# Kernel tuning notes

Hardware: AMD Instinct MI355X
Metric: run time of the kernel (lower is better)

## Reference

```python
import jax, jax.numpy as jnp
import numpy as np

B, S, D, NH, E, H, NT, K = 32, 512, 1024, 16, 16, 256, 8, 8
LN_EPS = 1e-5
W_MI = 5e-4


def setup_inputs() -> dict:
    key = jax.random.key(0)
    ks = jax.random.split(key, 12)
    p = lambda k, shape: jax.random.normal(k, shape, dtype=jnp.float32) * 0.02
    inp = {}
    inp["tgt"] = jax.random.normal(ks[0], (B, S, D), dtype=jnp.float32)
    inp["memory"] = jax.random.normal(ks[1], (B, S, D), dtype=jnp.float32)  # unused in norm_first path (faithful to source)
    inp["ln1_g"] = jnp.ones((D,), jnp.float32)
    inp["ln1_b"] = jnp.zeros((D,), jnp.float32)
    inp["ln3_g"] = jnp.ones((D,), jnp.float32)
    inp["ln3_b"] = jnp.zeros((D,), jnp.float32)
    inp["in_proj_w"] = p(ks[2], (3 * D, D))
    inp["in_proj_b"] = jnp.zeros((3 * D,), jnp.float32)
    inp["out_proj_w"] = p(ks[3], (D, D))
    inp["out_proj_b"] = jnp.zeros((D,), jnp.float32)
    inp["gate_w"] = p(ks[4], (NT, D, E))  # per-task gating Linear (no bias)
    inp["w1"] = p(ks[5], (E, D, H))
    inp["b1"] = jnp.zeros((E, H), jnp.float32)
    inp["w2"] = p(ks[6], (E, H, D))
    inp["b2"] = jnp.zeros((E, D), jnp.float32)
    inp["task_id"] = 3
    return inp


def _ln(x, g, b):
    m = x.mean(-1, keepdims=True)
    v = jnp.mean((x - m) ** 2, -1, keepdims=True)
    return (x - m) * jax.lax.rsqrt(v + LN_EPS) * g + b


def reference(tgt, memory, ln1_g, ln1_b, ln3_g, ln3_b, in_proj_w, in_proj_b,
              out_proj_w, out_proj_b, gate_w, w1, b1, w2, b2, task_id):
    dh = D // NH
    # --- pre-LN self-attention block ---
    h = _ln(tgt, ln1_g, ln1_b)
    qkv = h @ in_proj_w.T + in_proj_b  # [B,S,3D]
    q, k, v = jnp.split(qkv, 3, axis=-1)
    q = q.reshape(B, S, NH, dh)
    k = k.reshape(B, S, NH, dh)
    v = v.reshape(B, S, NH, dh)
    scores = jnp.einsum('bqhd,bkhd->bhqk', q, k) / jnp.sqrt(jnp.float32(dh))
    attn = jax.nn.softmax(scores, axis=-1)
    ctx = jnp.einsum('bhqk,bkhd->bqhd', attn, v).reshape(B, S, D)
    x = tgt + (ctx @ out_proj_w.T + out_proj_b)

    # --- task-conditioned MoE FFN (TaskMoE: per-task gate, top-k, GELU experts) ---
    h3 = _ln(x, ln3_g, ln3_b).reshape(B * S, D)  # [T,D]
    logits = h3 @ gate_w[task_id]  # [T,E]
    probs = jax.nn.softmax(logits, axis=-1)
    top_v, top_i = jax.lax.top_k(probs, K)
    gates = top_v / (top_v.sum(-1, keepdims=True) + 1e-6)
    gate_dense = jnp.einsum('tke,tk->te', jax.nn.one_hot(top_i, E, dtype=probs.dtype), gates)  # [T,E]
    u = jax.nn.gelu(jnp.einsum('td,edh->teh', h3, w1) + b1, approximate=False)  # [T,E,H]
    uw = u * gate_dense[:, :, None]
    moe = jnp.einsum('teh,ehd->td', uw, w2) + gate_dense @ b2  # [T,D]
    x = x + moe.reshape(B, S, D)

    mean_p = probs.mean(0)
    aux_loss = W_MI * jnp.sum(mean_p * jnp.log(mean_p + 1e-6))
    return (x, aux_loss, probs.reshape(B, S, E))
```

## Files before the change

kernel.cpp:

```cpp
#include <hip/hip_runtime.h>

typedef float f32x4 __attribute__((ext_vector_type(4)));
typedef _Float16 half_t;
typedef _Float16 h8 __attribute__((ext_vector_type(8)));
typedef _Float16 h4 __attribute__((ext_vector_type(4)));

__device__ __forceinline__ f32x4 mfma16(h8 a, h8 b, f32x4 c) {
  return __builtin_amdgcn_mfma_f32_16x16x32_f16(a, b, c, 0, 0, 0);
}

__global__ __launch_bounds__(256) void ln_fwd(const float* __restrict__ x,
                                              const float* __restrict__ g,
                                              const float* __restrict__ b,
                                              half_t* __restrict__ out) {
  const int row = blockIdx.x;
  const int tid = threadIdx.x;
  const float4 v = ((const float4*)(x + (size_t)row * 1024))[tid];
  float s = v.x + v.y + v.z + v.w;
  float q = v.x * v.x + v.y * v.y + v.z * v.z + v.w * v.w;
#pragma unroll
  for (int m = 1; m < 64; m <<= 1) { s += __shfl_xor(s, m); q += __shfl_xor(q, m); }
  __shared__ float red[8];
  const int wave = tid >> 6, lane = tid & 63;
  if (lane == 0) { red[wave] = s; red[wave + 4] = q; }
  __syncthreads();
  s = red[0] + red[1] + red[2] + red[3];
  q = red[4] + red[5] + red[6] + red[7];
  const float mean = s * (1.0f / 1024.0f);
  const float var = q * (1.0f / 1024.0f) - mean * mean;
  const float rstd = rsqrtf(var + 1e-5f);
  const float4 gv = ((const float4*)g)[tid];
  const float4 bv = ((const float4*)b)[tid];
  h4 o;
  o[0] = (half_t)((v.x - mean) * rstd * gv.x + bv.x);
  o[1] = (half_t)((v.y - mean) * rstd * gv.y + bv.y);
  o[2] = (half_t)((v.z - mean) * rstd * gv.z + bv.z);
  o[3] = (half_t)((v.w - mean) * rstd * gv.w + bv.w);
  *(h4*)(out + (size_t)row * 1024 + tid * 4) = o;
}

__global__ __launch_bounds__(256) void cvt_f2h(const float* __restrict__ in,
                                               half_t* __restrict__ out, int n) {
  const int i = (blockIdx.x * 256 + threadIdx.x) * 4;
  if (i < n) {
    const float4 v = *(const float4*)(in + i);
    h4 o = {(half_t)v.x, (half_t)v.y, (half_t)v.z, (half_t)v.w};
    *(h4*)(out + i) = o;
  }
}

__global__ __launch_bounds__(256) void tr_w1(const float* __restrict__ w1,
                                             half_t* __restrict__ w1t) {
  __shared__ float tile[32][33];
  const int e = blockIdx.z;
  const int tx = threadIdx.x & 31, ty = threadIdx.x >> 5;
  const int hh = blockIdx.x * 32 + tx;
#pragma unroll
  for (int i = 0; i < 4; ++i) {
    const int d = blockIdx.y * 32 + ty + i * 8;
    tile[ty + i * 8][tx] = w1[(size_t)e * 262144 + (size_t)d * 256 + hh];
  }
  __syncthreads();
#pragma unroll
  for (int i = 0; i < 4; ++i) {
    const int hho = blockIdx.x * 32 + ty + i * 8;
    const int k = blockIdx.y * 32 + tx;
    w1t[(size_t)(e * 256 + hho) * 1024 + k] = (half_t)tile[tx][ty + i * 8];
  }
}

__global__ __launch_bounds__(256) void tr_w2(const float* __restrict__ w2,
                                             half_t* __restrict__ w2t) {
  __shared__ float tile[32][33];
  const int e = blockIdx.z;
  const int tx = threadIdx.x & 31, ty = threadIdx.x >> 5;
  const int d_in = blockIdx.x * 32 + tx;
#pragma unroll
  for (int i = 0; i < 4; ++i) {
    const int hh = blockIdx.y * 32 + ty + i * 8;
    tile[ty + i * 8][tx] = w2[(size_t)e * 262144 + (size_t)hh * 1024 + d_in];
  }
  __syncthreads();
#pragma unroll
  for (int i = 0; i < 4; ++i) {
    const int d = blockIdx.x * 32 + ty + i * 8;
    const int hh = blockIdx.y * 32 + tx;
    w2t[(size_t)d * 4096 + e * 256 + hh] = (half_t)tile[tx][ty + i * 8];
  }
}

template <int EPI>
__global__ __launch_bounds__(512, 2) void gemm256(const half_t* __restrict__ A,
                                                  const half_t* __restrict__ Bt,
                                                  int N, int K, int nbx,
                                                  const float* __restrict__ bias,
                                                  const float* __restrict__ res,
                                                  const float* __restrict__ gd,
                                                  half_t* __restrict__ Ch,
                                                  float* __restrict__ Cf) {
  __shared__ half_t lds[2][2][256 * 64];
  const int tid = threadIdx.x;
  const int wave = tid >> 6, lane = tid & 63;
  const int l15 = lane & 15, g = lane >> 4;
  const int wr = wave >> 2, wc = wave & 3;

  const int nwg = gridDim.x;
  const int bid = blockIdx.x;
  const int swz = (bid & 7) * (nwg >> 3) + (bid >> 3);
  const int bx = swz % nbx, by = swz / nbx;

  const int NT = K >> 6;
  f32x4 acc[8][4] = {};

  auto stageAB = [&](int kt) {
    const int bt = kt & 1;
    const size_t abase = (size_t)(by * 256) * K + kt * 64;
    const size_t bbase = (size_t)(bx * 256) * K + kt * 64;
#pragma unroll
    for (int j = 0; j < 4; ++j) {
      const int c = tid + j * 512;
      const int row = c >> 3, sl = c & 7;
      const int col = (sl ^ (row & 7)) << 3;
      __builtin_amdgcn_global_load_lds(
          (const __attribute__((address_space(1))) void*)(A + abase + (size_t)row * K + col),
          (__attribute__((address_space(3))) void*)(&lds[bt][0][c * 8]), 16, 0, 0);
      __builtin_amdgcn_global_load_lds(
          (const __attribute__((address_space(1))) void*)(Bt + bbase + (size_t)row * K + col),
          (__attribute__((address_space(3))) void*)(&lds[bt][1][c * 8]), 16, 0, 0);
    }
  };

  stageAB(0);
  for (int kt = 0; kt < NT; ++kt) {
    const int bt = kt & 1;
    if (kt + 1 < NT) {
      stageAB(kt + 1);
      asm volatile("s_waitcnt vmcnt(8)" ::: "memory");
    } else {
      asm volatile("s_waitcnt vmcnt(0)" ::: "memory");
    }
    __builtin_amdgcn_s_barrier();

    h8 a0[4][2], a1[4][2], b0[2][2], b1[2][2];
#pragma unroll
    for (int m4 = 0; m4 < 4; ++m4)
#pragma unroll
      for (int kk = 0; kk < 2; ++kk) {
        const int row = wr * 128 + m4 * 16 + l15;
        const int sl = ((kk << 2) | g) ^ (row & 7);
        a0[m4][kk] = *(const h8*)(&lds[bt][0][row * 64 + sl * 8]);
      }
#pragma unroll
    for (int n2 = 0; n2 < 2; ++n2)
#pragma unroll
      for (int kk = 0; kk < 2; ++kk) {
        const int rowb0 = wc * 64 + n2 * 16 + l15;
        const int slb0 = ((kk << 2) | g) ^ (rowb0 & 7);
        b0[n2][kk] = *(const h8*)(&lds[bt][1][rowb0 * 64 + slb0 * 8]);
        const int rowb1 = wc * 64 + 32 + n2 * 16 + l15;
        const int slb1 = ((kk << 2) | g) ^ (rowb1 & 7);
        b1[n2][kk] = *(const h8*)(&lds[bt][1][rowb1 * 64 + slb1 * 8]);
      }
#pragma unroll
    for (int m4 = 0; m4 < 4; ++m4)
#pragma unroll
      for (int n2 = 0; n2 < 2; ++n2)
#pragma unroll
        for (int kk = 0; kk < 2; ++kk) {
          acc[m4][n2] = mfma16(a0[m4][kk], b0[n2][kk], acc[m4][n2]);
          acc[m4][2 + n2] = mfma16(a0[m4][kk], b1[n2][kk], acc[m4][2 + n2]);
        }
#pragma unroll
    for (int m4 = 0; m4 < 4; ++m4)
#pragma unroll
      for (int kk = 0; kk < 2; ++kk) {
        const int row = wr * 128 + 64 + m4 * 16 + l15;
        const int sl = ((kk << 2) | g) ^ (row & 7);
        a1[m4][kk] = *(const h8*)(&lds[bt][0][row * 64 + sl * 8]);
      }
#pragma unroll
    for (int m4 = 0; m4 < 4; ++m4)
#pragma unroll
      for (int n2 = 0; n2 < 2; ++n2)
#pragma unroll
        for (int kk = 0; kk < 2; ++kk) {
          acc[4 + m4][n2] = mfma16(a1[m4][kk], b0[n2][kk], acc[4 + m4][n2]);
          acc[4 + m4][2 + n2] = mfma16(a1[m4][kk], b1[n2][kk], acc[4 + m4][2 + n2]);
        }

    asm volatile("s_waitcnt lgkmcnt(0)" ::: "memory");
    __builtin_amdgcn_s_barrier();
  }

#pragma unroll
  for (int m = 0; m < 8; ++m) {
#pragma unroll
    for (int n = 0; n < 4; ++n) {
      const int col = bx * 256 + wc * 64 + n * 16 + l15;
      float bv = 0.0f;
      if constexpr (EPI != 3) bv = bias[col];
#pragma unroll
      for (int r = 0; r < 4; ++r) {
        const int row = by * 256 + wr * 128 + m * 16 + g * 4 + r;
        const float v = acc[m][n][r] + bv;
        if constexpr (EPI == 0) {
          Ch[(size_t)row * N + col] = (half_t)v;
        } else if constexpr (EPI == 1) {
          Cf[(size_t)row * N + col] = res[(size_t)row * N + col] + v;
        } else if constexpr (EPI == 2) {
          const float gel = 0.5f * v * (1.0f + erff(v * 0.70710678118f));
          Ch[(size_t)row * N + col] = (half_t)(gel * gd[row * 16 + (col >> 8)]);
        } else {
          Cf[(size_t)row * N + col] = res[(size_t)row * N + col] + v;
        }
      }
    }
  }
}

__global__ __launch_bounds__(256) void attn_fwd(const half_t* __restrict__ qkv,
                                                half_t* __restrict__ ctx) {
  const int bh = blockIdx.y;
  const int b = bh >> 4, h = bh & 15;
  const int qbase = blockIdx.x * 64;
  const int tid = threadIdx.x;
  const int wave = tid >> 6, lane = tid & 63;
  const int l15 = lane & 15, g = lane >> 4;
  __shared__ half_t K_s[2][32 * 64];
  __shared__ half_t Vt_s[2][64 * 32];
  __shared__ half_t P_s[4][16 * 32];

  const size_t qrow = (size_t)(b * 512 + qbase + wave * 16 + l15);
  h8 aq0 = *(const h8*)(qkv + qrow * 3072 + h * 64 + g * 8);
  h8 aq1 = *(const h8*)(qkv + qrow * 3072 + h * 64 + 32 + g * 8);
  aq0 = aq0 * (half_t)0.125f;
  aq1 = aq1 * (half_t)0.125f;

  float mr[4], sr[4];
  f32x4 o[4] = {};
#pragma unroll
  for (int r = 0; r < 4; ++r) { mr[r] = -1e30f; sr[r] = 0.0f; }

  const int key = tid >> 3, c0 = (tid & 7) << 3;
  const half_t* kbase = qkv + 1024 + h * 64 + c0;
  const half_t* vbase = qkv + 2048 + h * 64 + c0;

  for (int kt = 0; kt < 16; ++kt) {
    const int buf = kt & 1;
    const size_t krow = (size_t)(b * 512 + kt * 32 + key);
    const h8 kv = *(const h8*)(kbase + krow * 3072);
    *(h8*)(&K_s[buf][key * 64 + c0]) = kv;
    const h8 vv = *(const h8*)(vbase + krow * 3072);
#pragma unroll
    for (int j = 0; j < 8; ++j) Vt_s[buf][(c0 + j) * 32 + key] = vv[j];
    __syncthreads();

    f32x4 s0 = {0.f, 0.f, 0.f, 0.f}, s1 = {0.f, 0.f, 0.f, 0.f};
    s0 = mfma16(aq0, *(const h8*)(&K_s[buf][l15 * 64 + g * 8]), s0);
    s0 = mfma16(aq1, *(const h8*)(&K_s[buf][l15 * 64 + 32 + g * 8]), s0);
    s1 = mfma16(aq0, *(const h8*)(&K_s[buf][(16 + l15) * 64 + g * 8]), s1);
    s1 = mfma16(aq1, *(const h8*)(&K_s[buf][(16 + l15) * 64 + 32 + g * 8]), s1);

#pragma unroll
    for (int r = 0; r < 4; ++r) {
      const float a0 = s0[r], a1 = s1[r];
      float tm = fmaxf(a0, a1);
#pragma unroll
      for (int msk = 1; msk < 16; msk <<= 1) tm = fmaxf(tm, __shfl_xor(tm, msk));
      const float mnew = fmaxf(mr[r], tm);
      const float alpha = __expf(mr[r] - mnew);
      const float p0 = __expf(a0 - mnew), p1 = __expf(a1 - mnew);
      float rs = p0 + p1;
#pragma unroll
      for (int msk = 1; msk < 16; msk <<= 1) rs += __shfl_xor(rs, msk);
      sr[r] = sr[r] * alpha + rs;
      mr[r] = mnew;
#pragma unroll
      for (int d = 0; d < 4; ++d) o[d][r] *= alpha;
      P_s[wave][(g * 4 + r) * 32 + l15] = (half_t)p0;
      P_s[wave][(g * 4 + r) * 32 + 16 + l15] = (half_t)p1;
    }
    __syncthreads();

    const h8 pa = *(const h8*)(&P_s[wave][l15 * 32 + g * 8]);
#pragma unroll
    for (int d = 0; d < 4; ++d)
      o[d] = mfma16(pa, *(const h8*)(&Vt_s[buf][(d * 16 + l15) * 32 + g * 8]), o[d]);
  }
#pragma unroll
  for (int d = 0; d < 4; ++d) {
#pragma unroll
    for (int r = 0; r < 4; ++r) {
      const size_t row = (size_t)(b * 512 + qbase + wave * 16 + g * 4 + r);
      ctx[row * 1024 + h * 64 + d * 16 + l15] = (half_t)(o[d][r] / sr[r]);
    }
  }
}

__global__ __launch_bounds__(256) void gate_fwd(const half_t* __restrict__ h3,
                                                const float* __restrict__ gate_w,
                                                const int* __restrict__ task_id,
                                                float* __restrict__ probs,
                                                float* __restrict__ gd,
                                                float* __restrict__ mp) {
  const int tid = threadIdx.x, wave = tid >> 6, lane = tid & 63;
  const float* gw = gate_w + (size_t)task_id[0] * 16384;
  __shared__ float mp_part[16];
  if (tid < 16) mp_part[tid] = 0.0f;
  __syncthreads();
  float mpl[16];
#pragma unroll
  for (int e = 0; e < 16; ++e) mpl[e] = 0.0f;
  const int t0 = blockIdx.x * 64 + wave * 16;
  for (int tt = 0; tt < 16; ++tt) {
    const int t = t0 + tt;
    float acc[16];
#pragma unroll
    for (int e = 0; e < 16; ++e) acc[e] = 0.0f;
#pragma unroll
    for (int i = 0; i < 16; ++i) {
      const int d = i * 64 + lane;
      const float hv = (float)h3[(size_t)t * 1024 + d];
      const float4* gp = (const float4*)(gw + d * 16);
      const float4 g0 = gp[0], g1 = gp[1], g2 = gp[2], g3 = gp[3];
      acc[0] = fmaf(hv, g0.x, acc[0]);  acc[1] = fmaf(hv, g0.y, acc[1]);
      acc[2] = fmaf(hv, g0.z, acc[2]);  acc[3] = fmaf(hv, g0.w, acc[3]);
      acc[4] = fmaf(hv, g1.x, acc[4]);  acc[5] = fmaf(hv, g1.y, acc[5]);
      acc[6] = fmaf(hv, g1.z, acc[6]);  acc[7] = fmaf(hv, g1.w, acc[7]);
      acc[8] = fmaf(hv, g2.x, acc[8]);  acc[9] = fmaf(hv, g2.y, acc[9]);
      acc[10] = fmaf(hv, g2.z, acc[10]); acc[11] = fmaf(hv, g2.w, acc[11]);
      acc[12] = fmaf(hv, g3.x, acc[12]); acc[13] = fmaf(hv, g3.y, acc[13]);
      acc[14] = fmaf(hv, g3.z, acc[14]); acc[15] = fmaf(hv, g3.w, acc[15]);
    }
#pragma unroll
    for (int msk = 32; msk >= 1; msk >>= 1)
#pragma unroll
      for (int e = 0; e < 16; ++e) acc[e] += __shfl_xor(acc[e], msk);
    float mx = acc[0];
#pragma unroll
    for (int e = 1; e < 16; ++e) mx = fmaxf(mx, acc[e]);
    float p[16];
    float sum = 0.0f;
#pragma unroll
    for (int e = 0; e < 16; ++e) { p[e] = __expf(acc[e] - mx); sum += p[e]; }
    const float inv = 1.0f / sum;
#pragma unroll
    for (int e = 0; e < 16; ++e) p[e] *= inv;
    float myp = p[0];
#pragma unroll
    for (int e = 1; e < 16; ++e) myp = (lane == e) ? p[e] : myp;
    if (lane < 16) probs[(size_t)t * 16 + lane] = myp;
#pragma unroll
    for (int e = 0; e < 16; ++e) mpl[e] += p[e];
    float v[16];
#pragma unroll
    for (int e = 0; e < 16; ++e) v[e] = p[e];
    float topv[8];
    int topi[8];
#pragma unroll
    for (int k = 0; k < 8; ++k) {
      float vm = -1.0f;
      int im = 0;
#pragma unroll
      for (int e = 0; e < 16; ++e) {
        const bool gt = v[e] > vm;
        vm = gt ? v[e] : vm;
        im = gt ? e : im;
      }
      topv[k] = vm; topi[k] = im;
#pragma unroll
      for (int e = 0; e < 16; ++e) v[e] = (e == im) ? -1.0f : v[e];
    }
    float ts = 1e-6f;
#pragma unroll
    for (int k = 0; k < 8; ++k) ts += topv[k];
    const float tinv = 1.0f / ts;
    float gval = 0.0f;
#pragma unroll
    for (int k = 0; k < 8; ++k) gval = (topi[k] == lane) ? topv[k] * tinv : gval;
    if (lane < 16) gd[(size_t)t * 16 + lane] = gval;
  }
  if (lane == 0) {
#pragma unroll
    for (int e = 0; e < 16; ++e) atomicAdd(&mp_part[e], mpl[e]);
  }
  __syncthreads();
  if (tid < 16) atomicAdd(&mp[tid], mp_part[tid]);
}

__global__ void aux_fwd(const float* __restrict__ mp, float* __restrict__ out) {
  if (threadIdx.x == 0) {
    float a = 0.0f;
    for (int e = 0; e < 16; ++e) {
      const float m = mp[e] * (1.0f / 16384.0f);
      a += m * logf(m + 1e-6f);
    }
    out[0] = 5e-4f * a;
  }
}

__global__ __launch_bounds__(256) void bias2_add(const float* __restrict__ gd,
                                                 const float* __restrict__ b2,
                                                 float* __restrict__ out) {
  const int t = blockIdx.x, tid = threadIdx.x;
  __shared__ float gds[16];
  if (tid < 16) gds[tid] = gd[(size_t)t * 16 + tid];
  __syncthreads();
  float4 v = *(const float4*)(out + (size_t)t * 1024 + tid * 4);
#pragma unroll
  for (int e = 0; e < 16; ++e) {
    const float gv = gds[e];
    const float4 bv = *(const float4*)(b2 + e * 1024 + tid * 4);
    v.x = fmaf(gv, bv.x, v.x);
    v.y = fmaf(gv, bv.y, v.y);
    v.z = fmaf(gv, bv.z, v.z);
    v.w = fmaf(gv, bv.w, v.w);
  }
  *(float4*)(out + (size_t)t * 1024 + tid * 4) = v;
}

extern "C" void kernel_launch(void* const* d_in, const int* in_sizes, int n_in,
                              void* d_out, int out_size, void* d_ws, size_t ws_size,
                              hipStream_t stream) {
  const float* tgt = (const float*)d_in[0];
  const float* ln1_g = (const float*)d_in[2];
  const float* ln1_b = (const float*)d_in[3];
  const float* ln3_g = (const float*)d_in[4];
  const float* ln3_b = (const float*)d_in[5];
  const float* Wqkv = (const float*)d_in[6];
  const float* bqkv = (const float*)d_in[7];
  const float* Wout = (const float*)d_in[8];
  const float* bout = (const float*)d_in[9];
  const float* gate_w = (const float*)d_in[10];
  const float* w1 = (const float*)d_in[11];
  const float* b1 = (const float*)d_in[12];
  const float* w2 = (const float*)d_in[13];
  const float* b2 = (const float*)d_in[14];
  const int* task = (const int*)d_in[15];
  float* out = (float*)d_out;
  char* ws = (char*)d_ws;

  half_t* h = (half_t*)(ws + 0ull);
  half_t* qkv = (half_t*)(ws + 33554432ull);
  half_t* ctx = (half_t*)(ws + 134217728ull);
  half_t* uw = (half_t*)(ws + 33554432ull);
  half_t* wqkv_h = (half_t*)(ws + 167772160ull);
  half_t* wout_h = (half_t*)(ws + 174063616ull);
  half_t* w1t = (half_t*)(ws + 176160768ull);
  half_t* w2t = (half_t*)(ws + 184549376ull);
  float* gd = (float*)(ws + 192937984ull);
  float* mp = (float*)(ws + 193986560ull);

  hipMemsetAsync(mp, 0, 64, stream);
  cvt_f2h<<<3072, 256, 0, stream>>>(Wqkv, wqkv_h, 3145728);
  cvt_f2h<<<1024, 256, 0, stream>>>(Wout, wout_h, 1048576);
  tr_w1<<<dim3(8, 32, 16), 256, 0, stream>>>(w1, w1t);
  tr_w2<<<dim3(32, 8, 16), 256, 0, stream>>>(w2, w2t);

  ln_fwd<<<16384, 256, 0, stream>>>(tgt, ln1_g, ln1_b, h);
  gemm256<0><<<768, 512, 0, stream>>>(h, wqkv_h, 3072, 1024, 12, bqkv, nullptr, nullptr, qkv, nullptr);
  attn_fwd<<<dim3(8, 512), 256, 0, stream>>>(qkv, ctx);
  gemm256<1><<<256, 512, 0, stream>>>(ctx, wout_h, 1024, 1024, 4, bout, tgt, nullptr, nullptr, out);

  ln_fwd<<<16384, 256, 0, stream>>>(out, ln3_g, ln3_b, h);
  gate_fwd<<<256, 256, 0, stream>>>(h, gate_w, task, out + 16777217, gd, mp);
  aux_fwd<<<1, 64, 0, stream>>>(mp, out + 16777216);
  bias2_add<<<16384, 256, 0, stream>>>(gd, b2, out);
  gemm256<2><<<1024, 512, 0, stream>>>(h, w1t, 4096, 1024, 16, b1, nullptr, gd, uw, nullptr);
  gemm256<3><<<256, 512, 0, stream>>>(uw, w2t, 1024, 4096, 4, nullptr, out, nullptr, nullptr, out);
}
```

Baseline: 1.160 ms.

## Restructure attention with pre-transposed V, async LDS loads and larger tiles

Adds a separate kernel that transposes V per head into a contiguous buffer. Attention is rewritten to process 128 queries per block with 64-key tiles, using global_load_lds double buffering with XOR-swizzled LDS and an XCD-aware block mapping. The aim is to remove the scattered per-element V transpose stores and raise MFMA work per barrier. bias2_add now handles 16 tokens per block so the b2 loads are reused across tokens. The cost is an extra transpose pass and more register pressure in the attention kernel.

```diff
diff --git a/kernel.cpp b/kernel.cpp
--- a/kernel.cpp
+++ b/kernel.cpp
@@ -86,6 +86,27 @@
     const int d = blockIdx.x * 32 + ty + i * 8;
     const int hh = blockIdx.y * 32 + tx;
     w2t[(size_t)d * 4096 + e * 256 + hh] = (half_t)tile[tx][ty + i * 8];
+  }
+}
+
+__global__ __launch_bounds__(256) void tr_v(const half_t* __restrict__ qkv,
+                                            half_t* __restrict__ vt) {
+  __shared__ half_t tile[32][33];
+  const int bh = blockIdx.z;
+  const int b = bh >> 4, h = bh & 15;
+  const int st = blockIdx.x, dt = blockIdx.y;
+  const int tx = threadIdx.x & 31, ty = threadIdx.x >> 5;
+#pragma unroll
+  for (int i = 0; i < 4; ++i) {
+    const int s = st * 32 + ty + i * 8;
+    tile[ty + i * 8][tx] =
+        qkv[(size_t)(b * 512 + s) * 3072 + 2048 + h * 64 + dt * 32 + tx];
+  }
+  __syncthreads();
+#pragma unroll
+  for (int i = 0; i < 4; ++i) {
+    const int d = dt * 32 + ty + i * 8;
+    vt[((size_t)bh * 64 + d) * 512 + st * 32 + tx] = tile[tx][ty + i * 8];
   }
 }
 
@@ -219,82 +240,141 @@
 }
 
 __global__ __launch_bounds__(256) void attn_fwd(const half_t* __restrict__ qkv,
+                                                const half_t* __restrict__ vt,
                                                 half_t* __restrict__ ctx) {
-  const int bh = blockIdx.y;
-  const int b = bh >> 4, h = bh & 15;
-  const int qbase = blockIdx.x * 64;
+  __shared__ half_t K_s[2][64 * 64];
+  __shared__ half_t V_s[2][64 * 64];
+  __shared__ half_t P_s[4][32 * 72];
   const int tid = threadIdx.x;
   const int wave = tid >> 6, lane = tid & 63;
   const int l15 = lane & 15, g = lane >> 4;
-  __shared__ half_t K_s[2][32 * 64];
-  __shared__ half_t Vt_s[2][64 * 32];
-  __shared__ half_t P_s[4][16 * 32];
-
-  const size_t qrow = (size_t)(b * 512 + qbase + wave * 16 + l15);
-  h8 aq0 = *(const h8*)(qkv + qrow * 3072 + h * 64 + g * 8);
-  h8 aq1 = *(const h8*)(qkv + qrow * 3072 + h * 64 + 32 + g * 8);
-  aq0 = aq0 * (half_t)0.125f;
-  aq1 = aq1 * (half_t)0.125f;
-
-  float mr[4], sr[4];
-  f32x4 o[4] = {};
-#pragma unroll
-  for (int r = 0; r < 4; ++r) { mr[r] = -1e30f; sr[r] = 0.0f; }
-
-  const int key = tid >> 3, c0 = (tid & 7) << 3;
-  const half_t* kbase = qkv + 1024 + h * 64 + c0;
-  const half_t* vbase = qkv + 2048 + h * 64 + c0;
-
-  for (int kt = 0; kt < 16; ++kt) {
-    const int buf = kt & 1;
-    const size_t krow = (size_t)(b * 512 + kt * 32 + key);
-    const h8 kv = *(const h8*)(kbase + krow * 3072);
-    *(h8*)(&K_s[buf][key * 64 + c0]) = kv;
-    const h8 vv = *(const h8*)(vbase + krow * 3072);
-#pragma unroll
-    for (int j = 0; j < 8; ++j) Vt_s[buf][(c0 + j) * 32 + key] = vv[j];
-    __syncthreads();
-
-    f32x4 s0 = {0.f, 0.f, 0.f, 0.f}, s1 = {0.f, 0.f, 0.f, 0.f};
-    s0 = mfma16(aq0, *(const h8*)(&K_s[buf][l15 * 64 + g * 8]), s0);
-    s0 = mfma16(aq1, *(const h8*)(&K_s[buf][l15 * 64 + 32 + g * 8]), s0);
-    s1 = mfma16(aq0, *(const h8*)(&K_s[buf][(16 + l15) * 64 + g * 8]), s1);
-    s1 = mfma16(aq1, *(const h8*)(&K_s[buf][(16 + l15) * 64 + 32 + g * 8]), s1);
-
-#pragma unroll
-    for (int r = 0; r < 4; ++r) {
-      const float a0 = s0[r], a1 = s1[r];
-      float tm = fmaxf(a0, a1);
-#pragma unroll
-      for (int msk = 1; msk < 16; msk <<= 1) tm = fmaxf(tm, __shfl_xor(tm, msk));
-      const float mnew = fmaxf(mr[r], tm);
-      const float alpha = __expf(mr[r] - mnew);
-      const float p0 = __expf(a0 - mnew), p1 = __expf(a1 - mnew);
-      float rs = p0 + p1;
-#pragma unroll
-      for (int msk = 1; msk < 16; msk <<= 1) rs += __shfl_xor(rs, msk);
-      sr[r] = sr[r] * alpha + rs;
-      mr[r] = mnew;
-#pragma unroll
-      for (int d = 0; d < 4; ++d) o[d][r] *= alpha;
-      P_s[wave][(g * 4 + r) * 32 + l15] = (half_t)p0;
-      P_s[wave][(g * 4 + r) * 32 + 16 + l15] = (half_t)p1;
-    }
-    __syncthreads();
-
-    const h8 pa = *(const h8*)(&P_s[wave][l15 * 32 + g * 8]);
-#pragma unroll
-    for (int d = 0; d < 4; ++d)
-      o[d] = mfma16(pa, *(const h8*)(&Vt_s[buf][(d * 16 + l15) * 32 + g * 8]), o[d]);
-  }
-#pragma unroll
-  for (int d = 0; d < 4; ++d) {
-#pragma unroll
-    for (int r = 0; r < 4; ++r) {
-      const size_t row = (size_t)(b * 512 + qbase + wave * 16 + g * 4 + r);
-      ctx[row * 1024 + h * 64 + d * 16 + l15] = (half_t)(o[d][r] / sr[r]);
-    }
-  }
+
+  const int fid = blockIdx.x;
+  const int xcd = fid & 7, idx = fid >> 3;
+  const int bh = xcd * 64 + (idx >> 7) * 32 + (idx & 31);
+  const int qt = (idx >> 5) & 3;
+  const int b = bh >> 4, h = bh & 15;
+
+  h8 qreg[2][2];
+#pragma unroll
+  for (int m = 0; m < 2; ++m) {
+    const size_t qrow = (size_t)(b * 512 + qt * 128 + wave * 32 + m * 16 + l15);
+#pragma unroll
+    for (int kk = 0; kk < 2; ++kk) {
+      h8 t = *(const h8*)(qkv + qrow * 3072 + h * 64 + kk * 32 + g * 8);
+      qreg[m][kk] = t * (half_t)0.125f;
+    }
+  }
+
+  float mr[2][4], sr[2][4];
+  f32x4 o[2][4] = {};
+#pragma unroll
+  for (int m = 0; m < 2; ++m)
+#pragma unroll
+    for (int r = 0; r < 4; ++r) { mr[m][r] = -1e30f; sr[m][r] = 0.0f; }
+
+  const half_t* kg = qkv + (size_t)(b * 512) * 3072 + 1024 + h * 64;
+  const half_t* vg = vt + (size_t)bh * 32768;
+
+  auto stage = [&](int kt) {
+    const int bt = kt & 1;
+#pragma unroll
+    for (int j = 0; j < 2; ++j) {
+      const int s = tid + j * 256;
+      const int row = s >> 3, sl = s & 7;
+      const int col = (sl ^ (row & 7)) << 3;
+      __builtin_amdgcn_global_load_lds(
+          (const __attribute__((address_space(1))) void*)(kg + (size_t)(kt * 64 + row) * 3072 + col),
+          (__attribute__((address_space(3))) void*)(&K_s[bt][s * 8]), 16, 0, 0);
+      __builtin_amdgcn_global_load_lds(
+          (const __attribute__((address_space(1))) void*)(vg + (size_t)row * 512 + kt * 64 + col),
+          (__attribute__((address_space(3))) void*)(&V_s[bt][s * 8]), 16, 0, 0);
+    }
+  };
+
+  stage(0);
+  for (int kt = 0; kt < 8; ++kt) {
+    const int bt = kt & 1;
+    if (kt < 7) {
+      stage(kt + 1);
+      asm volatile("s_waitcnt vmcnt(4)" ::: "memory");
+    } else {
+      asm volatile("s_waitcnt vmcnt(0)" ::: "memory");
+    }
+    __builtin_amdgcn_s_barrier();
+
+    f32x4 s_acc[2][4] = {};
+    h8 bk[4][2];
+#pragma unroll
+    for (int n = 0; n < 4; ++n)
+#pragma unroll
+      for (int kk = 0; kk < 2; ++kk)
+        bk[n][kk] = *(const h8*)(&K_s[bt][(n * 16 + l15) * 64 + (((kk * 4 + g) ^ (l15 & 7)) << 3)]);
+#pragma unroll
+    for (int m = 0; m < 2; ++m)
+#pragma unroll
+      for (int n = 0; n < 4; ++n)
+#pragma unroll
+        for (int kk = 0; kk < 2; ++kk)
+          s_acc[m][n] = mfma16(qreg[m][kk], bk[n][kk], s_acc[m][n]);
+
+#pragma unroll
+    for (int m = 0; m < 2; ++m)
+#pragma unroll
+      for (int r = 0; r < 4; ++r) {
+        float tm = fmaxf(fmaxf(s_acc[m][0][r], s_acc[m][1][r]),
+                         fmaxf(s_acc[m][2][r], s_acc[m][3][r]));
+#pragma unroll
+        for (int msk = 1; msk < 16; msk <<= 1) tm = fmaxf(tm, __shfl_xor(tm, msk));
+        const float mnew = fmaxf(mr[m][r], tm);
+        const float al = __expf(mr[m][r] - mnew);
+        mr[m][r] = mnew;
+        float rs = 0.0f;
+#pragma unroll
+        for (int n = 0; n < 4; ++n) {
+          const float p = __expf(s_acc[m][n][r] - mnew);
+          rs += p;
+          P_s[wave][(m * 16 + g * 4 + r) * 72 + n * 16 + l15] = (half_t)p;
+        }
+#pragma unroll
+        for (int msk = 1; msk < 16; msk <<= 1) rs += __shfl_xor(rs, msk);
+        sr[m][r] = sr[m][r] * al + rs;
+#pragma unroll
+        for (int d = 0; d < 4; ++d) o[m][d][r] *= al;
+      }
+
+    h8 bv[4][2], pa[2][2];
+#pragma unroll
+    for (int n = 0; n < 4; ++n)
+#pragma unroll
+      for (int kk = 0; kk < 2; ++kk)
+        bv[n][kk] = *(const h8*)(&V_s[bt][(n * 16 + l15) * 64 + (((kk * 4 + g) ^ (l15 & 7)) << 3)]);
+#pragma unroll
+    for (int m = 0; m < 2; ++m)
+#pragma unroll
+      for (int kk = 0; kk < 2; ++kk)
+        pa[m][kk] = *(const h8*)(&P_s[wave][(m * 16 + l15) * 72 + kk * 32 + g * 8]);
+#pragma unroll
+    for (int m = 0; m < 2; ++m)
+#pragma unroll
+      for (int n = 0; n < 4; ++n)
+#pragma unroll
+        for (int kk = 0; kk < 2; ++kk)
+          o[m][n] = mfma16(pa[m][kk], bv[n][kk], o[m][n]);
+
+    asm volatile("s_waitcnt lgkmcnt(0)" ::: "memory");
+    __builtin_amdgcn_s_barrier();
+  }
+
+#pragma unroll
+  for (int m = 0; m < 2; ++m)
+#pragma unroll
+    for (int n = 0; n < 4; ++n)
+#pragma unroll
+      for (int r = 0; r < 4; ++r) {
+        const size_t row = (size_t)(b * 512 + qt * 128 + wave * 32 + m * 16 + g * 4 + r);
+        ctx[row * 1024 + h * 64 + n * 16 + l15] = (half_t)(o[m][n][r] / sr[m][r]);
+      }
 }
 
 __global__ __launch_bounds__(256) void gate_fwd(const half_t* __restrict__ h3,
@@ -402,21 +482,26 @@
 __global__ __launch_bounds__(256) void bias2_add(const float* __restrict__ gd,
                                                  const float* __restrict__ b2,
                                                  float* __restrict__ out) {
-  const int t = blockIdx.x, tid = threadIdx.x;
-  __shared__ float gds[16];
-  if (tid < 16) gds[tid] = gd[(size_t)t * 16 + tid];
-  __syncthreads();
-  float4 v = *(const float4*)(out + (size_t)t * 1024 + tid * 4);
-#pragma unroll
-  for (int e = 0; e < 16; ++e) {
-    const float gv = gds[e];
-    const float4 bv = *(const float4*)(b2 + e * 1024 + tid * 4);
-    v.x = fmaf(gv, bv.x, v.x);
-    v.y = fmaf(gv, bv.y, v.y);
-    v.z = fmaf(gv, bv.z, v.z);
-    v.w = fmaf(gv, bv.w, v.w);
-  }
-  *(float4*)(out + (size_t)t * 1024 + tid * 4) = v;
+  const int t0 = blockIdx.x * 16;
+  const int tid = threadIdx.x;
+  __shared__ float gds[16][16];
+  gds[tid >> 4][tid & 15] = gd[(size_t)(t0 + (tid >> 4)) * 16 + (tid & 15)];
+  __syncthreads();
+  float4 bv[16];
+#pragma unroll
+  for (int e = 0; e < 16; ++e) bv[e] = *(const float4*)(b2 + e * 1024 + tid * 4);
+  for (int tt = 0; tt < 16; ++tt) {
+    float4 v = *(const float4*)(out + (size_t)(t0 + tt) * 1024 + tid * 4);
+#pragma unroll
+    for (int e = 0; e < 16; ++e) {
+      const float gv = gds[tt][e];
+      v.x = fmaf(gv, bv[e].x, v.x);
+      v.y = fmaf(gv, bv[e].y, v.y);
+      v.z = fmaf(gv, bv[e].z, v.z);
+      v.w = fmaf(gv, bv[e].w, v.w);
+    }
+    *(float4*)(out + (size_t)(t0 + tt) * 1024 + tid * 4) = v;
+  }
 }
 
 extern "C" void kernel_launch(void* const* d_in, const int* in_sizes, int n_in,
@@ -441,6 +526,7 @@
   char* ws = (char*)d_ws;
 
   half_t* h = (half_t*)(ws + 0ull);
+  half_t* vt = (half_t*)(ws + 0ull);
   half_t* qkv = (half_t*)(ws + 33554432ull);
   half_t* ctx = (half_t*)(ws + 134217728ull);
   half_t* uw = (half_t*)(ws + 33554432ull);
@@ -459,13 +545,14 @@
 
   ln_fwd<<<16384, 256, 0, stream>>>(tgt, ln1_g, ln1_b, h);
   gemm256<0><<<768, 512, 0, stream>>>(h, wqkv_h, 3072, 1024, 12, bqkv, nullptr, nullptr, qkv, nullptr);
-  attn_fwd<<<dim3(8, 512), 256, 0, stream>>>(qkv, ctx);
+  tr_v<<<dim3(16, 2, 512), 256, 0, stream>>>(qkv, vt);
+  attn_fwd<<<2048, 256, 0, stream>>>(qkv, vt, ctx);
   gemm256<1><<<256, 512, 0, stream>>>(ctx, wout_h, 1024, 1024, 4, bout, tgt, nullptr, nullptr, out);
 
   ln_fwd<<<16384, 256, 0, stream>>>(out, ln3_g, ln3_b, h);
   gate_fwd<<<256, 256, 0, stream>>>(h, gate_w, task, out + 16777217, gd, mp);
   aux_fwd<<<1, 64, 0, stream>>>(mp, out + 16777216);
-  bias2_add<<<16384, 256, 0, stream>>>(gd, b2, out);
+  bias2_add<<<1024, 256, 0, stream>>>(gd, b2, out);
   gemm256<2><<<1024, 512, 0, stream>>>(h, w1t, 4096, 1024, 16, b1, nullptr, gd, uw, nullptr);
   gemm256<3><<<256, 512, 0, stream>>>(uw, w2t, 1024, 4096, 4, nullptr, out, nullptr, nullptr, out);
 }
```

Result: faster. 1.069 ms (-7.9%).
